# Kernel tuning notes

Measured on AMD Instinct MI355X. Metric: run time of the kernel, lower is better.

Reference implementation:

```python
import jax, jax.numpy as jnp
import numpy as np

D_MODEL = 768
D_STATE = 64
D_CONV = 4
EXPAND = 2
D_INNER = D_MODEL * EXPAND
BATCH = 2
SEQ = 1024
LN_EPS = 1e-5


def setup_inputs() -> dict:
    key = jax.random.key(0)
    ks = jax.random.split(key, 8)
    s = lambda k, shape, scale=0.02: (jax.random.normal(k, shape, jnp.float32) * scale)
    x = jax.random.normal(ks[0], (BATCH, SEQ, D_MODEL), jnp.float32)
    return {
        "x": x,
        "ln_w": jnp.ones((D_MODEL,), jnp.float32),
        "ln_b": jnp.zeros((D_MODEL,), jnp.float32),
        "in_proj_w": s(ks[1], (D_MODEL, 2 * D_INNER)),            # x @ W, torch Linear weight transposed
        "conv_w": s(ks[2], (D_INNER, 1, D_CONV), 0.1),            # depthwise (O, I/groups=1, K)
        "conv_b": jnp.zeros((D_INNER,), jnp.float32),
        "x_proj_w": s(ks[3], (D_INNER, 2 * D_STATE + 1)),
        "A_log": jnp.log(jnp.arange(1, D_STATE + 1, dtype=jnp.float32)),
        "D": jnp.ones((D_INNER,), jnp.float32),
        "dt_w": s(ks[4], (1, D_INNER), 0.5),
        "dt_b": s(ks[5], (D_INNER,), 0.1),
        "out_proj_w": s(ks[6], (D_INNER, D_MODEL)),
    }


def reference(x, ln_w, ln_b, in_proj_w, conv_w, conv_b, x_proj_w, A_log, D, dt_w, dt_b, out_proj_w):
    residual = x
    # LayerNorm
    mu = jnp.mean(x, axis=-1, keepdims=True)
    var = jnp.mean((x - mu) ** 2, axis=-1, keepdims=True)
    h = (x - mu) * jax.lax.rsqrt(var + LN_EPS) * ln_w + ln_b
    # input projection -> (main, gate)
    xz = h @ in_proj_w                                   # (B, L, 2*d_inner)
    x_main, z = jnp.split(xz, 2, axis=-1)
    # causal depthwise conv1d: torch pads (d_conv-1) both sides then truncates to L == left-pad only
    xc = jax.lax.conv_general_dilated(
        x_main.transpose(0, 2, 1), conv_w,
        window_strides=(1,), padding=[(D_CONV - 1, 0)],
        feature_group_count=D_INNER,
        dimension_numbers=("NCH", "OIH", "NCH"))
    xc = (xc + conv_b[None, :, None]).transpose(0, 2, 1)  # (B, L, d_inner)
    xc = jax.nn.silu(xc)
    # input-dependent SSM params
    proj = xc @ x_proj_w                                  # (B, L, 2*d_state+1)
    Bm = proj[..., :D_STATE]
    Cm = proj[..., D_STATE:2 * D_STATE]
    dt = jax.nn.softplus(proj[..., -1:] @ dt_w + dt_b)    # (B, L, d_inner)
    A = -jnp.exp(A_log)                                   # (d_state,)

    def step(h_prev, inp):
        x_t, dt_t, B_t, C_t = inp                         # (B,d_inner),(B,d_inner),(B,d_state),(B,d_state)
        dA = jnp.exp(A[None, None, :] * dt_t[..., None])  # (B, d_inner, d_state)
        h_new = dA * h_prev + (dt_t * x_t)[..., None] * B_t[:, None, :]
        y_t = jnp.einsum("bds,bs->bd", h_new, C_t)
        return h_new, y_t

    h0 = jnp.zeros((x.shape[0], D_INNER, D_STATE), xc.dtype)
    xs = (xc.transpose(1, 0, 2), dt.transpose(1, 0, 2),
          Bm.transpose(1, 0, 2), Cm.transpose(1, 0, 2))
    _, ys = jax.lax.scan(step, h0, xs)                    # ys: (L, B, d_inner)
    y = ys.transpose(1, 0, 2)
    y = y + D * xc
    y = y * jax.nn.silu(z)
    y = y @ out_proj_w                                    # (B, L, d_model)
    return y + residual
```

## Files before the change

kernel.cpp:

```cpp
#include <hip/hip_runtime.h>
#include <hip/hip_bf16.h>
#include <cstdint>
#include <cstddef>

#define D_MODEL   768
#define D_INNER   1536
#define D_STATE   64
#define NBATCH    2
#define SEQ       1024
#define NROWS     (NBATCH*SEQ)
#define NCHUNK    32
#define TCHUNK    32
#define PROJ_LD   132
#define BD_TOT    (NBATCH*D_INNER)
#define RPB       4

#define L2E 1.4426950408889634f
#define LN2 0.6931471805599453f

typedef __bf16 bf16x8 __attribute__((ext_vector_type(8)));
typedef float  f32x4  __attribute__((ext_vector_type(4)));

__device__ __forceinline__ float fexp2(float x){ return __builtin_amdgcn_exp2f(x); }
__device__ __forceinline__ float flog2(float x){ return __builtin_amdgcn_logf(x); }
__device__ __forceinline__ float softplus_f(float x){
  float r = LN2 * flog2(1.0f + fexp2(x * L2E));
  return x > 15.0f ? x : r;
}
__device__ __forceinline__ float silu_f(float x){
  return x / (1.0f + fexp2(-x * L2E));
}

__device__ __forceinline__ void gload_lds16(const void* g, void* l){
  __builtin_amdgcn_global_load_lds(
      (const __attribute__((address_space(1))) void*)g,
      (__attribute__((address_space(3))) void*)l, 16, 0, 0);
}

#define T1_TILES 2304
#define T3_TILES 1152
#define T2_TILES 192
#define TP_TOTAL (T1_TILES+T3_TILES+T2_TILES)

__global__ __launch_bounds__(256) void prep_all_kernel(
    const float* __restrict__ in_proj, const float* __restrict__ out_proj,
    const float* __restrict__ x_proj, const float* __restrict__ x,
    const float* __restrict__ ln_w, const float* __restrict__ ln_b,
    __bf16* __restrict__ WT1, __bf16* __restrict__ WT3,
    __bf16* __restrict__ WT2, __bf16* __restrict__ h_ln,
    float* __restrict__ proj, float* __restrict__ out,
    float* __restrict__ wdtc){
  __shared__ float shbuf[32*33];
  const int blk = blockIdx.x;
  if (blk < TP_TOTAL){
    const float* W; __bf16* WT; int K, ldw, tiles_x, idx;
    if (blk < T1_TILES){ W = in_proj; WT = WT1; K = D_MODEL; ldw = 2*D_INNER; tiles_x = 96; idx = blk; }
    else if (blk < T1_TILES+T3_TILES){ W = out_proj; WT = WT3; K = D_INNER; ldw = D_MODEL; tiles_x = 24; idx = blk - T1_TILES; }
    else { W = x_proj; WT = WT2; K = D_INNER; ldw = 129; tiles_x = 4; idx = blk - T1_TILES - T3_TILES; }
    const int n0 = (idx % tiles_x) * 32, k0 = (idx / tiles_x) * 32;
    const int tx = threadIdx.x, ty = threadIdx.y;
    float (*tile)[33] = (float(*)[33])shbuf;
    #pragma unroll
    for (int i = ty; i < 32; i += 8)
      tile[i][tx] = W[(size_t)(k0 + i) * ldw + n0 + tx];
    __syncthreads();
    #pragma unroll
    for (int i = ty; i < 32; i += 8)
      WT[(size_t)(n0 + i) * K + k0 + tx] = (__bf16)tile[tx][i];
  } else if (blk < TP_TOTAL + NROWS){
    const int row = blk - TP_TOTAL;
    const float* xr = x + (size_t)row * D_MODEL;
    const int tid = threadIdx.y * 32 + threadIdx.x;
    float v0 = xr[tid], v1 = xr[tid+256], v2 = xr[tid+512];
    float s  = v0+v1+v2;
    float ss = v0*v0+v1*v1+v2*v2;
    #pragma unroll
    for (int off = 32; off > 0; off >>= 1){
      s  += __shfl_down(s, off);
      ss += __shfl_down(ss, off);
    }
    float* red = shbuf;
    const int wv = tid >> 6, ln = tid & 63;
    if (ln == 0){ red[wv] = s; red[4+wv] = ss; }
    __syncthreads();
    if (tid == 0){
      float S  = red[0]+red[1]+red[2]+red[3];
      float SS = red[4]+red[5]+red[6]+red[7];
      float mu = S * (1.0f/D_MODEL);
      float var = SS * (1.0f/D_MODEL) - mu*mu;
      red[0] = mu;
      red[1] = rsqrtf(var + 1e-5f);
    }
    __syncthreads();
    float mu = red[0], inv = red[1];
    __bf16* orow = h_ln + (size_t)row * D_MODEL;
    orow[tid]     = (__bf16)((v0 - mu)*inv*ln_w[tid]     + ln_b[tid]);
    orow[tid+256] = (__bf16)((v1 - mu)*inv*ln_w[tid+256] + ln_b[tid+256]);
    orow[tid+512] = (__bf16)((v2 - mu)*inv*ln_w[tid+512] + ln_b[tid+512]);
    float* og = out + (size_t)row * D_MODEL;
    og[tid]     = v0;
    og[tid+256] = v1;
    og[tid+512] = v2;
    if (tid < 128) proj[(size_t)row * PROJ_LD + tid] = 0.0f;
  } else {
    const int tid = threadIdx.y * 32 + threadIdx.x;
    #pragma unroll
    for (int k = 0; k < 6; ++k){
      int d = tid + k*256;
      wdtc[d] = x_proj[(size_t)d*129 + 128];
    }
  }
}

struct SMem {
  __bf16 sA[128][32];
  __bf16 sB[128][32];
};

template<int MODE>
__device__ __forceinline__ void gemm_tile(
    const __bf16* __restrict__ A, const __bf16* __restrict__ Bt,
    float* __restrict__ Cf, __bf16* __restrict__ Cb,
    int lda, int ldb, int ldc, int m0, int n0, int kbeg, int kend,
    SMem& sm, int tid){
  const int wave = tid >> 6;
  const int lane = tid & 63;
  const int quad = lane >> 4;
  const int l16  = lane & 15;
  const int wm = (wave >> 1) * 64;
  const int wn = (wave & 1) * 64;
  const int srow = lane >> 2;
  const int scol = (lane & 3) * 8;

  f32x4 acc[4][4] = {};
  for (int k0 = kbeg; k0 < kend; k0 += 32){
    #pragma unroll
    for (int p = 0; p < 2; ++p){
      int r = wave*32 + p*16 + srow;
      gload_lds16(A  + (size_t)(m0 + r)*lda + k0 + scol, &sm.sA[wave*32 + p*16][0]);
      gload_lds16(Bt + (size_t)(n0 + r)*ldb + k0 + scol, &sm.sB[wave*32 + p*16][0]);
    }
    __syncthreads();
    bf16x8 af[4], bfr[4];
    #pragma unroll
    for (int i = 0; i < 4; ++i) af[i]  = *(const bf16x8*)&sm.sA[wm + i*16 + l16][quad*8];
    #pragma unroll
    for (int j = 0; j < 4; ++j) bfr[j] = *(const bf16x8*)&sm.sB[wn + j*16 + l16][quad*8];
    #pragma unroll
    for (int i = 0; i < 4; ++i)
      #pragma unroll
      for (int j = 0; j < 4; ++j)
        acc[i][j] = __builtin_amdgcn_mfma_f32_16x16x32_bf16(af[i], bfr[j], acc[i][j], 0, 0, 0);
    __syncthreads();
  }
  #pragma unroll
  for (int i = 0; i < 4; ++i)
    #pragma unroll
    for (int j = 0; j < 4; ++j)
      #pragma unroll
      for (int r = 0; r < 4; ++r){
        int row = m0 + wm + i*16 + quad*4 + r;
        int col = n0 + wn + j*16 + l16;
        size_t off = (size_t)row * ldc + col;
        if (MODE == 2)      atomicAdd(&Cf[off], acc[i][j][r]);
        else if (MODE == 1) Cb[off] = (__bf16)acc[i][j][r];
        else                Cf[off] = acc[i][j][r];
      }
}

struct Args {
  const __bf16* h_ln; const __bf16* WT1; const __bf16* WT2; const __bf16* WT3;
  const float* conv_w; const float* conv_b;
  const float* dt_w; const float* dt_b; const float* Dp;
  const float* wdtc;
  float* xz;
  __bf16* zb;
  __bf16* xcb; float* proj;
  float* dtv; float* dtx;
  float* sdtA; __bf16* Lb; __bf16* ybf; float* out;
};

__global__ __launch_bounds__(256) void k_gemm1(Args a){
  __shared__ SMem sm;
  const int bx = blockIdx.x;
  if (bx < 12)
    gemm_tile<0>(a.h_ln, a.WT1, a.xz, nullptr, D_MODEL, D_MODEL, D_INNER,
                 blockIdx.y*128, bx*128, 0, D_MODEL, sm, threadIdx.x);
  else
    gemm_tile<1>(a.h_ln, a.WT1 + (size_t)D_INNER*D_MODEL, nullptr, a.zb,
                 D_MODEL, D_MODEL, D_INNER,
                 blockIdx.y*128, (bx-12)*128, 0, D_MODEL, sm, threadIdx.x);
}

__global__ __launch_bounds__(256) void k_conv(Args a){
  __shared__ float red[4];
  const int r0  = blockIdx.x * RPB;
  const int tid = threadIdx.x;
  const int t0  = r0 & (SEQ-1);
  float4 w4[6]; float cb[6], wdt[6], dw[6], db[6];
  float x1[6], x2[6], x3[6];
  #pragma unroll
  for (int q = 0; q < 6; ++q){
    const int d = tid + q*256;
    w4[q]  = *(const float4*)(a.conv_w + (size_t)d*4);
    cb[q]  = a.conv_b[d];
    wdt[q] = a.wdtc[d];
    dw[q]  = a.dt_w[d];
    db[q]  = a.dt_b[d];
    x1[q] = (t0 >= 1) ? a.xz[(size_t)(r0-1)*D_INNER + d] : 0.0f;
    x2[q] = (t0 >= 2) ? a.xz[(size_t)(r0-2)*D_INNER + d] : 0.0f;
    x3[q] = (t0 >= 3) ? a.xz[(size_t)(r0-3)*D_INNER + d] : 0.0f;
  }
  for (int tl = 0; tl < RPB; ++tl){
    const int row = r0 + tl;
    float v[6]; float dtpart = 0.0f;
    #pragma unroll
    for (int q = 0; q < 6; ++q){
      const int d = tid + q*256;
      float x0 = a.xz[(size_t)row*D_INNER + d];
      float acc = cb[q];
      acc = fmaf(x3[q], w4[q].x, acc);
      acc = fmaf(x2[q], w4[q].y, acc);
      acc = fmaf(x1[q], w4[q].z, acc);
      acc = fmaf(x0,    w4[q].w, acc);
      float vv = silu_f(acc);
      v[q] = vv;
      a.xcb[(size_t)row*D_INNER + d] = (__bf16)vv;
      dtpart = fmaf(vv, wdt[q], dtpart);
      x3[q] = x2[q]; x2[q] = x1[q]; x1[q] = x0;
    }
    #pragma unroll
    for (int off = 32; off > 0; off >>= 1) dtpart += __shfl_down(dtpart, off);
    if ((tid & 63) == 0) red[tid >> 6] = dtpart;
    __syncthreads();
    const float draw = red[0]+red[1]+red[2]+red[3];
    __syncthreads();
    #pragma unroll
    for (int q = 0; q < 6; ++q){
      const int d = tid + q*256;
      float dv = softplus_f(fmaf(draw, dw[q], db[q]));
      a.dtv[(size_t)row*D_INNER + d] = dv;
      a.dtx[(size_t)row*D_INNER + d] = dv * v[q];
    }
  }
}

__global__ __launch_bounds__(256) void k_xproj(Args a){
  __shared__ SMem sm;
  const int kz = blockIdx.x;
  const int m0 = blockIdx.y * 128;
  gemm_tile<2>(a.xcb, a.WT2, a.proj, nullptr, D_INNER, D_INNER, PROJ_LD,
               m0, 0, kz*384, kz*384+384, sm, threadIdx.x);
}


__global__ __launch_bounds__(128) void k_scanA(Args a){
  const int bd = blockIdx.x * 128 + threadIdx.x;
  const int c  = blockIdx.y;
  const int b  = __builtin_amdgcn_readfirstlane(bd / D_INNER);
  const int d  = bd - b * D_INNER;
  float h[D_STATE];
  #pragma unroll
  for (int n = 0; n < D_STATE; ++n) h[n] = 0.0f;
  float sdt = 0.0f;
  #pragma unroll 2
  for (int tl = 0; tl < TCHUNK; ++tl){
    const int row = b*SEQ + c*TCHUNK + tl;
    const float* Brow = a.proj + (size_t)row * PROJ_LD;
    float dtv = a.dtv[(size_t)row * D_INNER + d];
    float dtx = a.dtx[(size_t)row * D_INNER + d];
    sdt += dtv;
    float r1 = fexp2(-L2E * dtv);
    float r2 = r1*r1, r4 = r2*r2, r8 = r4*r4;
    float p0=r1, p1=r2, p2=r1*r2, p3=r4, p4=r1*r4, p5=r2*r4, p6=r1*r2*r4, p7=r8;
    #pragma unroll
    for (int n = 0; n < D_STATE; n += 8){
      h[n]   = fmaf(p0, h[n],   dtx * Brow[n]);
      h[n+1] = fmaf(p1, h[n+1], dtx * Brow[n+1]);
      h[n+2] = fmaf(p2, h[n+2], dtx * Brow[n+2]);
      h[n+3] = fmaf(p3, h[n+3], dtx * Brow[n+3]);
      h[n+4] = fmaf(p4, h[n+4], dtx * Brow[n+4]);
      h[n+5] = fmaf(p5, h[n+5], dtx * Brow[n+5]);
      h[n+6] = fmaf(p6, h[n+6], dtx * Brow[n+6]);
      h[n+7] = fmaf(p7, h[n+7], dtx * Brow[n+7]);
      if (n + 8 < D_STATE){
        p0*=r8; p1*=r8; p2*=r8; p3*=r8; p4*=r8; p5*=r8; p6*=r8; p7*=r8;
      }
    }
  }
  a.sdtA[(size_t)c * BD_TOT + bd] = sdt;
  #pragma unroll
  for (int n = 0; n < D_STATE; ++n)
    a.Lb[((size_t)c * D_STATE + n) * BD_TOT + bd] = (__bf16)h[n];
}

__global__ __launch_bounds__(256) void k_scanB(Args a){
  const int bd = blockIdx.x * 256 + threadIdx.x;
  const int n  = blockIdx.y;
  const float k2n = -(float)(n+1) * L2E;
  float h = 0.0f;
  #pragma unroll 4
  for (int c = 0; c < NCHUNK; ++c){
    float sdt = a.sdtA[(size_t)c * BD_TOT + bd];
    float P = fexp2(k2n * sdt);
    size_t adr = ((size_t)c * D_STATE + n) * BD_TOT + bd;
    float L = (float)a.Lb[adr];
    a.Lb[adr] = (__bf16)h;
    h = fmaf(P, h, L);
  }
}

__global__ __launch_bounds__(128) void k_scanC(Args a){
  const int bd = blockIdx.x * 128 + threadIdx.x;
  const int c  = blockIdx.y;
  const int b  = __builtin_amdgcn_readfirstlane(bd / D_INNER);
  const int d  = bd - b * D_INNER;
  const float Dd = a.Dp[d];
  float h[D_STATE];
  #pragma unroll
  for (int n = 0; n < D_STATE; ++n)
    h[n] = (float)a.Lb[((size_t)c * D_STATE + n) * BD_TOT + bd];
  #pragma unroll 2
  for (int tl = 0; tl < TCHUNK; ++tl){
    const int row = b*SEQ + c*TCHUNK + tl;
    const float* Brow = a.proj + (size_t)row * PROJ_LD;
    const float* Crow = Brow + D_STATE;
    float dtv = a.dtv[(size_t)row * D_INNER + d];
    float dtx = a.dtx[(size_t)row * D_INNER + d];
    float xcv = (float)a.xcb[(size_t)row * D_INNER + d];
    float r1 = fexp2(-L2E * dtv);
    float r2 = r1*r1, r4 = r2*r2, r8 = r4*r4;
    float p0=r1, p1=r2, p2=r1*r2, p3=r4, p4=r1*r4, p5=r2*r4, p6=r1*r2*r4, p7=r8;
    float y0=0.f, y1=0.f, y2=0.f, y3=0.f;
    #pragma unroll
    for (int n = 0; n < D_STATE; n += 8){
      h[n]   = fmaf(p0, h[n],   dtx * Brow[n]);   y0 = fmaf(h[n],   Crow[n],   y0);
      h[n+1] = fmaf(p1, h[n+1], dtx * Brow[n+1]); y1 = fmaf(h[n+1], Crow[n+1], y1);
      h[n+2] = fmaf(p2, h[n+2], dtx * Brow[n+2]); y2 = fmaf(h[n+2], Crow[n+2], y2);
      h[n+3] = fmaf(p3, h[n+3], dtx * Brow[n+3]); y3 = fmaf(h[n+3], Crow[n+3], y3);
      h[n+4] = fmaf(p4, h[n+4], dtx * Brow[n+4]); y0 = fmaf(h[n+4], Crow[n+4], y0);
      h[n+5] = fmaf(p5, h[n+5], dtx * Brow[n+5]); y1 = fmaf(h[n+5], Crow[n+5], y1);
      h[n+6] = fmaf(p6, h[n+6], dtx * Brow[n+6]); y2 = fmaf(h[n+6], Crow[n+6], y2);
      h[n+7] = fmaf(p7, h[n+7], dtx * Brow[n+7]); y3 = fmaf(h[n+7], Crow[n+7], y3);
      if (n + 8 < D_STATE){
        p0*=r8; p1*=r8; p2*=r8; p3*=r8; p4*=r8; p5*=r8; p6*=r8; p7*=r8;
      }
    }
    float y = (y0 + y1) + (y2 + y3);
    float zv = (float)a.zb[(size_t)row * D_INNER + d];
    float yv = (y + Dd * xcv) * silu_f(zv);
    a.ybf[(size_t)row * D_INNER + d] = (__bf16)yv;
  }
}

__global__ __launch_bounds__(256) void k_gemm2(Args a){
  __shared__ SMem sm;
  const int kz = blockIdx.x & 3;
  const int n0 = (blockIdx.x >> 2) * 128;
  const int m0 = blockIdx.y * 128;
  gemm_tile<2>(a.ybf, a.WT3, a.out, nullptr, D_INNER, D_INNER, D_MODEL,
               m0, n0, kz*384, kz*384+384, sm, threadIdx.x);
}

extern "C" void kernel_launch(void* const* d_in, const int* in_sizes, int n_in,
                              void* d_out, int out_size, void* d_ws, size_t ws_size,
                              hipStream_t stream){
  const float* x        = (const float*)d_in[0];
  const float* ln_w     = (const float*)d_in[1];
  const float* ln_b     = (const float*)d_in[2];
  const float* in_proj  = (const float*)d_in[3];
  const float* conv_w   = (const float*)d_in[4];
  const float* conv_b   = (const float*)d_in[5];
  const float* x_proj   = (const float*)d_in[6];
  const float* A_log    = (const float*)d_in[7];  (void)A_log;
  const float* Dp       = (const float*)d_in[8];
  const float* dt_w     = (const float*)d_in[9];
  const float* dt_b     = (const float*)d_in[10];
  const float* out_proj = (const float*)d_in[11];
  float* out = (float*)d_out;

  char* p = (char*)d_ws;
  size_t used = 0;
  auto alloc = [&](size_t bytes) -> char* {
    char* r = p + used;
    used += (bytes + 255) & ~(size_t)255;
    return r;
  };
  __bf16* h_ln = (__bf16*)alloc((size_t)NROWS*D_MODEL*sizeof(__bf16));
  __bf16* WT1  = (__bf16*)alloc((size_t)(2*D_INNER)*D_MODEL*sizeof(__bf16));
  __bf16* WT3  = (__bf16*)alloc((size_t)D_MODEL*D_INNER*sizeof(__bf16));
  __bf16* WT2  = (__bf16*)alloc((size_t)128*D_INNER*sizeof(__bf16));
  __bf16* ybf  = (__bf16*)alloc((size_t)NROWS*D_INNER*sizeof(__bf16));
  __bf16* xcb  = (__bf16*)alloc((size_t)NROWS*D_INNER*sizeof(__bf16));
  __bf16* zb   = (__bf16*)alloc((size_t)NROWS*D_INNER*sizeof(__bf16));
  float*  xz   = (float*)alloc((size_t)NROWS*D_INNER*sizeof(float));
  float*  proj = (float*)alloc((size_t)NROWS*PROJ_LD*sizeof(float));
  float*  dtv  = (float*)alloc((size_t)NROWS*D_INNER*sizeof(float));
  float*  dtx  = (float*)alloc((size_t)NROWS*D_INNER*sizeof(float));
  float*  sdtA = (float*)alloc((size_t)NCHUNK*BD_TOT*sizeof(float));
  float*  wdtc = (float*)alloc((size_t)D_INNER*sizeof(float));
  __bf16* Lb   = (__bf16*)alloc((size_t)NCHUNK*D_STATE*BD_TOT*sizeof(__bf16));
  if (used > ws_size) return;

  Args a;
  a.h_ln = h_ln; a.WT1 = WT1; a.WT2 = WT2; a.WT3 = WT3;
  a.conv_w = conv_w; a.conv_b = conv_b;
  a.dt_w = dt_w; a.dt_b = dt_b; a.Dp = Dp; a.wdtc = wdtc;
  a.xz = xz; a.zb = zb; a.xcb = xcb; a.proj = proj;
  a.dtv = dtv; a.dtx = dtx; a.sdtA = sdtA; a.Lb = Lb; a.ybf = ybf; a.out = out;

  hipLaunchKernelGGL(prep_all_kernel, dim3(TP_TOTAL + NROWS + 1), dim3(32,8), 0, stream,
                     in_proj, out_proj, x_proj, x, ln_w, ln_b, WT1, WT3, WT2, h_ln,
                     proj, out, wdtc);
  hipLaunchKernelGGL(k_gemm1, dim3(24, 16), dim3(256), 0, stream, a);
  hipLaunchKernelGGL(k_conv,  dim3(NROWS/RPB), dim3(256), 0, stream, a);
  hipLaunchKernelGGL(k_xproj, dim3(4, 16),  dim3(256), 0, stream, a);
  hipLaunchKernelGGL(k_scanA, dim3(24, NCHUNK), dim3(128), 0, stream, a);
  hipLaunchKernelGGL(k_scanB, dim3(12, D_STATE), dim3(256), 0, stream, a);
  hipLaunchKernelGGL(k_scanC, dim3(24, NCHUNK), dim3(128), 0, stream, a);
  hipLaunchKernelGGL(k_gemm2, dim3(24, 16), dim3(256), 0, stream, a);
}
```

Baseline: 252.0 us.

## Split scan state dimension across four threads per channel in scanA and scanC

The chunked scan kernels now give each thread 16 of the 64 state entries instead of all 64, with a per-quarter decay offset and a cross-lane shuffle reduction of y in scanC. This cuts register pressure and raises occupancy and parallelism, so the latency-bound recurrences have more waves in flight. The cost is redundant dt/exp work per quarter and extra shuffles. The conv kernel also prefetches the next row's input, and restrict pointers are added throughout.

```diff
diff --git a/kernel.cpp b/kernel.cpp
--- a/kernel.cpp
+++ b/kernel.cpp
@@ -197,8 +197,12 @@
   const int r0  = blockIdx.x * RPB;
   const int tid = threadIdx.x;
   const int t0  = r0 & (SEQ-1);
+  const float* __restrict__ xz   = a.xz;
+  __bf16* __restrict__ xcb       = a.xcb;
+  float* __restrict__ dtvp       = a.dtv;
+  float* __restrict__ dtxp       = a.dtx;
   float4 w4[6]; float cb[6], wdt[6], dw[6], db[6];
-  float x1[6], x2[6], x3[6];
+  float x1[6], x2[6], x3[6], nx[6];
   #pragma unroll
   for (int q = 0; q < 6; ++q){
     const int d = tid + q*256;
@@ -207,27 +211,35 @@
     wdt[q] = a.wdtc[d];
     dw[q]  = a.dt_w[d];
     db[q]  = a.dt_b[d];
-    x1[q] = (t0 >= 1) ? a.xz[(size_t)(r0-1)*D_INNER + d] : 0.0f;
-    x2[q] = (t0 >= 2) ? a.xz[(size_t)(r0-2)*D_INNER + d] : 0.0f;
-    x3[q] = (t0 >= 3) ? a.xz[(size_t)(r0-3)*D_INNER + d] : 0.0f;
+    x1[q] = (t0 >= 1) ? xz[(size_t)(r0-1)*D_INNER + d] : 0.0f;
+    x2[q] = (t0 >= 2) ? xz[(size_t)(r0-2)*D_INNER + d] : 0.0f;
+    x3[q] = (t0 >= 3) ? xz[(size_t)(r0-3)*D_INNER + d] : 0.0f;
+    nx[q] = xz[(size_t)r0*D_INNER + d];
   }
   for (int tl = 0; tl < RPB; ++tl){
     const int row = r0 + tl;
+    float x0[6];
+    #pragma unroll
+    for (int q = 0; q < 6; ++q) x0[q] = nx[q];
+    if (tl + 1 < RPB){
+      #pragma unroll
+      for (int q = 0; q < 6; ++q)
+        nx[q] = xz[(size_t)(row+1)*D_INNER + tid + q*256];
+    }
     float v[6]; float dtpart = 0.0f;
     #pragma unroll
     for (int q = 0; q < 6; ++q){
       const int d = tid + q*256;
-      float x0 = a.xz[(size_t)row*D_INNER + d];
       float acc = cb[q];
       acc = fmaf(x3[q], w4[q].x, acc);
       acc = fmaf(x2[q], w4[q].y, acc);
       acc = fmaf(x1[q], w4[q].z, acc);
-      acc = fmaf(x0,    w4[q].w, acc);
+      acc = fmaf(x0[q], w4[q].w, acc);
       float vv = silu_f(acc);
       v[q] = vv;
-      a.xcb[(size_t)row*D_INNER + d] = (__bf16)vv;
+      xcb[(size_t)row*D_INNER + d] = (__bf16)vv;
       dtpart = fmaf(vv, wdt[q], dtpart);
-      x3[q] = x2[q]; x2[q] = x1[q]; x1[q] = x0;
+      x3[q] = x2[q]; x2[q] = x1[q]; x1[q] = x0[q];
     }
     #pragma unroll
     for (int off = 32; off > 0; off >>= 1) dtpart += __shfl_down(dtpart, off);
@@ -239,8 +251,8 @@
     for (int q = 0; q < 6; ++q){
       const int d = tid + q*256;
       float dv = softplus_f(fmaf(draw, dw[q], db[q]));
-      a.dtv[(size_t)row*D_INNER + d] = dv;
-      a.dtx[(size_t)row*D_INNER + d] = dv * v[q];
+      dtvp[(size_t)row*D_INNER + d] = dv;
+      dtxp[(size_t)row*D_INNER + d] = dv * v[q];
     }
   }
 }
@@ -254,27 +266,35 @@
 }
 
 
-__global__ __launch_bounds__(128) void k_scanA(Args a){
-  const int bd = blockIdx.x * 128 + threadIdx.x;
+__global__ __launch_bounds__(256, 6) void k_scanA(Args a){
+  const int q  = blockIdx.x & 3;
+  const int cg = blockIdx.x >> 2;
+  const int bd = cg * 256 + threadIdx.x;
   const int c  = blockIdx.y;
-  const int b  = __builtin_amdgcn_readfirstlane(bd / D_INNER);
-  const int d  = bd - b * D_INNER;
-  float h[D_STATE];
+  const int b  = bd >= D_INNER;
+  const float* __restrict__ projp = a.proj;
+  const float* __restrict__ dtvp  = a.dtv;
+  const float* __restrict__ dtxp  = a.dtx;
+  float h[16];
   #pragma unroll
-  for (int n = 0; n < D_STATE; ++n) h[n] = 0.0f;
+  for (int n = 0; n < 16; ++n) h[n] = 0.0f;
   float sdt = 0.0f;
-  #pragma unroll 2
   for (int tl = 0; tl < TCHUNK; ++tl){
     const int row = b*SEQ + c*TCHUNK + tl;
-    const float* Brow = a.proj + (size_t)row * PROJ_LD;
-    float dtv = a.dtv[(size_t)row * D_INNER + d];
-    float dtx = a.dtx[(size_t)row * D_INNER + d];
+    const float* Brow = projp + (size_t)row * PROJ_LD + q*16;
+    float dtv = dtvp[(size_t)row * D_INNER + bd - b*D_INNER + b*D_INNER];
+    float dtx = dtxp[(size_t)row * D_INNER + bd - b*D_INNER + b*D_INNER];
     sdt += dtv;
     float r1 = fexp2(-L2E * dtv);
     float r2 = r1*r1, r4 = r2*r2, r8 = r4*r4;
-    float p0=r1, p1=r2, p2=r1*r2, p3=r4, p4=r1*r4, p5=r2*r4, p6=r1*r2*r4, p7=r8;
-    #pragma unroll
-    for (int n = 0; n < D_STATE; n += 8){
+    float base = 1.0f;
+    if (q == 1){ base = r8*r8; }
+    else if (q == 2){ float r16 = r8*r8; base = r16*r16; }
+    else if (q == 3){ float r16 = r8*r8; base = r16*r16*r16; }
+    float p0=r1*base, p1=r2*base, p2=r1*r2*base, p3=r4*base,
+          p4=r1*r4*base, p5=r2*r4*base, p6=r1*r2*r4*base, p7=r8*base;
+    #pragma unroll
+    for (int n = 0; n < 16; n += 8){
       h[n]   = fmaf(p0, h[n],   dtx * Brow[n]);
       h[n+1] = fmaf(p1, h[n+1], dtx * Brow[n+1]);
       h[n+2] = fmaf(p2, h[n+2], dtx * Brow[n+2]);
@@ -283,73 +303,102 @@
       h[n+5] = fmaf(p5, h[n+5], dtx * Brow[n+5]);
       h[n+6] = fmaf(p6, h[n+6], dtx * Brow[n+6]);
       h[n+7] = fmaf(p7, h[n+7], dtx * Brow[n+7]);
-      if (n + 8 < D_STATE){
+      if (n == 0){
         p0*=r8; p1*=r8; p2*=r8; p3*=r8; p4*=r8; p5*=r8; p6*=r8; p7*=r8;
       }
     }
   }
-  a.sdtA[(size_t)c * BD_TOT + bd] = sdt;
+  if (q == 0) a.sdtA[(size_t)c * BD_TOT + bd] = sdt;
+  __bf16* __restrict__ Lbp = a.Lb;
   #pragma unroll
-  for (int n = 0; n < D_STATE; ++n)
-    a.Lb[((size_t)c * D_STATE + n) * BD_TOT + bd] = (__bf16)h[n];
+  for (int n = 0; n < 16; ++n)
+    Lbp[((size_t)c * D_STATE + q*16 + n) * BD_TOT + bd] = (__bf16)h[n];
 }
 
 __global__ __launch_bounds__(256) void k_scanB(Args a){
   const int bd = blockIdx.x * 256 + threadIdx.x;
   const int n  = blockIdx.y;
   const float k2n = -(float)(n+1) * L2E;
+  const float* __restrict__ sdtp = a.sdtA;
+  __bf16* __restrict__ Lbp = a.Lb;
   float h = 0.0f;
   #pragma unroll 4
   for (int c = 0; c < NCHUNK; ++c){
-    float sdt = a.sdtA[(size_t)c * BD_TOT + bd];
+    float sdt = sdtp[(size_t)c * BD_TOT + bd];
     float P = fexp2(k2n * sdt);
     size_t adr = ((size_t)c * D_STATE + n) * BD_TOT + bd;
-    float L = (float)a.Lb[adr];
-    a.Lb[adr] = (__bf16)h;
+    float L = (float)Lbp[adr];
+    Lbp[adr] = (__bf16)h;
     h = fmaf(P, h, L);
   }
 }
 
-__global__ __launch_bounds__(128) void k_scanC(Args a){
-  const int bd = blockIdx.x * 128 + threadIdx.x;
-  const int c  = blockIdx.y;
-  const int b  = __builtin_amdgcn_readfirstlane(bd / D_INNER);
-  const int d  = bd - b * D_INNER;
+__global__ __launch_bounds__(256, 4) void k_scanC(Args a){
+  const int tid  = threadIdx.x;
+  const int wave = tid >> 6;
+  const int lane = tid & 63;
+  const int q    = lane >> 4;
+  const int ch   = lane & 15;
+  const int bd   = blockIdx.x * 64 + wave*16 + ch;
+  const int c    = blockIdx.y;
+  const int b    = bd >= D_INNER;
+  const int d    = bd - b * D_INNER;
+  const float* __restrict__ projp = a.proj;
+  const float* __restrict__ dtvp  = a.dtv;
+  const float* __restrict__ dtxp  = a.dtx;
+  const __bf16* __restrict__ xcbp = a.xcb;
+  const __bf16* __restrict__ zbp  = a.zb;
+  const __bf16* __restrict__ Lbp  = a.Lb;
+  __bf16* __restrict__ ybfp       = a.ybf;
   const float Dd = a.Dp[d];
-  float h[D_STATE];
+  float h[16];
   #pragma unroll
-  for (int n = 0; n < D_STATE; ++n)
-    h[n] = (float)a.Lb[((size_t)c * D_STATE + n) * BD_TOT + bd];
-  #pragma unroll 2
+  for (int n = 0; n < 16; ++n)
+    h[n] = (float)Lbp[((size_t)c * D_STATE + q*16 + n) * BD_TOT + bd];
   for (int tl = 0; tl < TCHUNK; ++tl){
     const int row = b*SEQ + c*TCHUNK + tl;
-    const float* Brow = a.proj + (size_t)row * PROJ_LD;
-    const float* Crow = Brow + D_STATE;
-    float dtv = a.dtv[(size_t)row * D_INNER + d];
-    float dtx = a.dtx[(size_t)row * D_INNER + d];
-    float xcv = (float)a.xcb[(size_t)row * D_INNER + d];
+    const float* Brow = projp + (size_t)row * PROJ_LD + q*16;
+    f32x4 Bv[4], Cv[4];
+    #pragma unroll
+    for (int i = 0; i < 4; ++i){
+      Bv[i] = *(const f32x4*)(Brow + i*4);
+      Cv[i] = *(const f32x4*)(Brow + 64 + i*4);
+    }
+    float dtv = dtvp[(size_t)row * D_INNER + d];
+    float dtx = dtxp[(size_t)row * D_INNER + d];
     float r1 = fexp2(-L2E * dtv);
     float r2 = r1*r1, r4 = r2*r2, r8 = r4*r4;
-    float p0=r1, p1=r2, p2=r1*r2, p3=r4, p4=r1*r4, p5=r2*r4, p6=r1*r2*r4, p7=r8;
+    float r16 = r8*r8;
+    float base = (q & 1) ? r16 : 1.0f;
+    float r32 = r16*r16;
+    if (q & 2) base *= r32;
+    float p0=r1*base, p1=r2*base, p2=r1*r2*base, p3=r4*base,
+          p4=r1*r4*base, p5=r2*r4*base, p6=r1*r2*r4*base, p7=r8*base;
     float y0=0.f, y1=0.f, y2=0.f, y3=0.f;
     #pragma unroll
-    for (int n = 0; n < D_STATE; n += 8){
-      h[n]   = fmaf(p0, h[n],   dtx * Brow[n]);   y0 = fmaf(h[n],   Crow[n],   y0);
-      h[n+1] = fmaf(p1, h[n+1], dtx * Brow[n+1]); y1 = fmaf(h[n+1], Crow[n+1], y1);
-      h[n+2] = fmaf(p2, h[n+2], dtx * Brow[n+2]); y2 = fmaf(h[n+2], Crow[n+2], y2);
-      h[n+3] = fmaf(p3, h[n+3], dtx * Brow[n+3]); y3 = fmaf(h[n+3], Crow[n+3], y3);
-      h[n+4] = fmaf(p4, h[n+4], dtx * Brow[n+4]); y0 = fmaf(h[n+4], Crow[n+4], y0);
-      h[n+5] = fmaf(p5, h[n+5], dtx * Brow[n+5]); y1 = fmaf(h[n+5], Crow[n+5], y1);
-      h[n+6] = fmaf(p6, h[n+6], dtx * Brow[n+6]); y2 = fmaf(h[n+6], Crow[n+6], y2);
-      h[n+7] = fmaf(p7, h[n+7], dtx * Brow[n+7]); y3 = fmaf(h[n+7], Crow[n+7], y3);
-      if (n + 8 < D_STATE){
+    for (int g = 0; g < 2; ++g){
+      const int n = g*8;
+      h[n]   = fmaf(p0, h[n],   dtx * Bv[g*2][0]);   y0 = fmaf(h[n],   Cv[g*2][0],   y0);
+      h[n+1] = fmaf(p1, h[n+1], dtx * Bv[g*2][1]);   y1 = fmaf(h[n+1], Cv[g*2][1],   y1);
+      h[n+2] = fmaf(p2, h[n+2], dtx * Bv[g*2][2]);   y2 = fmaf(h[n+2], Cv[g*2][2],   y2);
+      h[n+3] = fmaf(p3, h[n+3], dtx * Bv[g*2][3]);   y3 = fmaf(h[n+3], Cv[g*2][3],   y3);
+      h[n+4] = fmaf(p4, h[n+4], dtx * Bv[g*2+1][0]); y0 = fmaf(h[n+4], Cv[g*2+1][0], y0);
+      h[n+5] = fmaf(p5, h[n+5], dtx * Bv[g*2+1][1]); y1 = fmaf(h[n+5], Cv[g*2+1][1], y1);
+      h[n+6] = fmaf(p6, h[n+6], dtx * Bv[g*2+1][2]); y2 = fmaf(h[n+6], Cv[g*2+1][2], y2);
+      h[n+7] = fmaf(p7, h[n+7], dtx * Bv[g*2+1][3]); y3 = fmaf(h[n+7], Cv[g*2+1][3], y3);
+      if (g == 0){
         p0*=r8; p1*=r8; p2*=r8; p3*=r8; p4*=r8; p5*=r8; p6*=r8; p7*=r8;
       }
     }
     float y = (y0 + y1) + (y2 + y3);
-    float zv = (float)a.zb[(size_t)row * D_INNER + d];
-    float yv = (y + Dd * xcv) * silu_f(zv);
-    a.ybf[(size_t)row * D_INNER + d] = (__bf16)yv;
+    y += __shfl_xor(y, 16);
+    y += __shfl_xor(y, 32);
+    if (q == 0){
+      float xcv = (float)xcbp[(size_t)row * D_INNER + d];
+      float zv  = (float)zbp[(size_t)row * D_INNER + d];
+      float yv = (y + Dd * xcv) * silu_f(zv);
+      ybfp[(size_t)row * D_INNER + d] = (__bf16)yv;
+    }
   }
 }
 
@@ -415,8 +464,8 @@
   hipLaunchKernelGGL(k_gemm1, dim3(24, 16), dim3(256), 0, stream, a);
   hipLaunchKernelGGL(k_conv,  dim3(NROWS/RPB), dim3(256), 0, stream, a);
   hipLaunchKernelGGL(k_xproj, dim3(4, 16),  dim3(256), 0, stream, a);
-  hipLaunchKernelGGL(k_scanA, dim3(24, NCHUNK), dim3(128), 0, stream, a);
+  hipLaunchKernelGGL(k_scanA, dim3(48, NCHUNK), dim3(256), 0, stream, a);
   hipLaunchKernelGGL(k_scanB, dim3(12, D_STATE), dim3(256), 0, stream, a);
-  hipLaunchKernelGGL(k_scanC, dim3(24, NCHUNK), dim3(128), 0, stream, a);
+  hipLaunchKernelGGL(k_scanC, dim3(48, NCHUNK), dim3(256), 0, stream, a);
   hipLaunchKernelGGL(k_gemm2, dim3(24, 16), dim3(256), 0, stream, a);
 }
```

Measured after the change: 268.0 us. 6.3% more time.
